# Kernel optimization log

Hardware: AMD Instinct MI355X
Metric: run time of the kernel (lower is better)

Reference implementation:

```python
import jax, jax.numpy as jnp
import numpy as np

H, E, DFF = 768, 8, 3072
B, S = 2, 1024


def setup_inputs() -> dict:
    key = jax.random.key(0)
    ks = jax.random.split(key, 4)
    scale = 1.0 / np.sqrt(H)
    return {
        "x": jax.random.normal(ks[0], (B, S, H), dtype=jnp.float32),
        "Wg": jax.random.normal(ks[1], (H, E), dtype=jnp.float32) * scale,
        "bg": jnp.zeros((E,), dtype=jnp.float32),
        "W1": jax.random.normal(ks[2], (E, H, DFF), dtype=jnp.float32) * scale,
        "b1": jnp.zeros((E, DFF), dtype=jnp.float32),
        "W2": jax.random.normal(ks[3], (E, DFF, H), dtype=jnp.float32) * (1.0 / np.sqrt(DFF)),
        "b2": jnp.zeros((E, H), dtype=jnp.float32),
        "top_k": 2,
    }


def reference(x, Wg, bg, W1, b1, W2, b2, top_k):
    b, s, h = x.shape
    xf = x.reshape(-1, h)                       # [T, H]
    logits = xf @ Wg + bg                        # [T, E]
    probs = jax.nn.softmax(logits, axis=-1)
    w, idx = jax.lax.top_k(probs, top_k)         # [T, K]
    w = w / jnp.sum(w, axis=-1, keepdims=True)   # renormalize top-k weights
    # dense combine weights per (token, expert): [T, E]
    comb = jnp.sum(jax.nn.one_hot(idx, W1.shape[0], dtype=xf.dtype) * w[..., None], axis=1)
    # per-expert MLP: Linear -> exact GELU -> Linear
    hmid = jax.nn.gelu(jnp.einsum('th,ehf->etf', xf, W1) + b1[:, None, :], approximate=False)
    eo = jnp.einsum('etf,efh->eth', hmid, W2) + b2[:, None, :]   # [E, T, H]
    out = jnp.einsum('te,eth->th', comb, eo)     # weighted combine
    return out.reshape(b, s, h)
```

## Files before the change

kernel.cpp:

```cpp
#include <hip/hip_runtime.h>
#include <hip/hip_bf16.h>
#include <math.h>

#define H_DIM 768
#define E_NUM 8
#define DFF   3072
#define T_NUM 2048
#define PAIRS 4096

typedef __attribute__((ext_vector_type(8))) short          s16x8;
typedef __attribute__((ext_vector_type(4))) float          f32x4;
typedef __attribute__((ext_vector_type(4))) unsigned int   u32x4;
typedef __attribute__((ext_vector_type(4))) unsigned short u16x4;
typedef __attribute__((ext_vector_type(8))) unsigned short u16x8;

__device__ __forceinline__ unsigned short f2bf(float f) {
  unsigned int u = __builtin_bit_cast(unsigned int, f);
  u += 0x7FFFu + ((u >> 16) & 1u);
  return (unsigned short)(u >> 16);
}

__device__ __forceinline__ float bf2f(unsigned short v) {
  unsigned int u = ((unsigned int)v) << 16;
  return __builtin_bit_cast(float, u);
}

__device__ __forceinline__ float gelu_fast(float x) {
  float t = x * x;
  float a = __builtin_fmaf(t, -0.10294221f, -2.3022082f);
  float w;
  asm("v_exp_f32 %0, %1" : "=v"(w) : "v"(x * a));
  float r;
  float d = 1.0f + w;
  asm("v_rcp_f32 %0, %1" : "=v"(r) : "v"(d));
  return x * r;
}


__device__ __forceinline__ void route_body(
    int rb, const float* __restrict__ x, const float* __restrict__ Wg,
    const float* __restrict__ bg, int* __restrict__ eidx, float* __restrict__ ew) {
  int wave = threadIdx.x >> 6, lane = threadIdx.x & 63;
  int t = rb * 4 + wave;
  const float* xr = x + (size_t)t * H_DIM;
  float acc[E_NUM];
#pragma unroll
  for (int e = 0; e < E_NUM; ++e) acc[e] = 0.f;
#pragma unroll
  for (int i = 0; i < H_DIM / 64; ++i) {
    int h = i * 64 + lane;
    float xv = xr[h];
    f32x4 w0 = *(const f32x4*)&Wg[h * 8];
    f32x4 w1 = *(const f32x4*)&Wg[h * 8 + 4];
    acc[0] += xv * w0[0]; acc[1] += xv * w0[1];
    acc[2] += xv * w0[2]; acc[3] += xv * w0[3];
    acc[4] += xv * w1[0]; acc[5] += xv * w1[1];
    acc[6] += xv * w1[2]; acc[7] += xv * w1[3];
  }
#pragma unroll
  for (int e = 0; e < E_NUM; ++e) {
#pragma unroll
    for (int off = 32; off > 0; off >>= 1) acc[e] += __shfl_xor(acc[e], off);
  }
  if (lane == 0) {
    float l[E_NUM];
#pragma unroll
    for (int e = 0; e < E_NUM; ++e) l[e] = acc[e] + bg[e];
    int i0 = 0;
#pragma unroll
    for (int e = 1; e < E_NUM; ++e) if (l[e] > l[i0]) i0 = e;
    int i1 = (i0 == 0) ? 1 : 0;
#pragma unroll
    for (int e = 0; e < E_NUM; ++e) if (e != i0 && l[e] > l[i1]) i1 = e;
    float d  = expf(l[i1] - l[i0]);
    eidx[2 * t]     = i0;
    eidx[2 * t + 1] = i1;
    ew[2 * t]       = 1.f / (1.f + d);
    ew[2 * t + 1]   = d / (1.f + d);
  }
}

__device__ __forceinline__ void transpose_body(
    int tb, const float* __restrict__ in, unsigned short* __restrict__ out,
    int R, int C) {
  __shared__ unsigned short tile[128][136];
  int tpe = (R / 128) * (C / 128);
  int e   = tb / tpe;
  int rem = tb % tpe;
  int bx  = rem % (C / 128);
  int by  = rem / (C / 128);
  int c0 = bx * 128, r0 = by * 128;
  const float* ip = in + (size_t)e * R * C;
  unsigned short* op = out + (size_t)e * R * C;
  int tid = threadIdx.x;

  int tx = tid & 31, ty = tid >> 5;
#pragma unroll
  for (int i = 0; i < 16; ++i) {
    int r = i * 8 + ty;
    f32x4 v = *(const f32x4*)&ip[(size_t)(r0 + r) * C + c0 + tx * 4];
    u16x4 o;
    o[0] = f2bf(v[0]); o[1] = f2bf(v[1]); o[2] = f2bf(v[2]); o[3] = f2bf(v[3]);
    int cs = (tx * 4) ^ (((r >> 3) & 7) << 2);
    *(u16x4*)&tile[r][cs] = o;
  }
  __syncthreads();

  int rb2 = (tid & 15) * 8;
  int key = (tid & 7) << 2;
#pragma unroll
  for (int p = 0; p < 8; ++p) {
    int c = p * 16 + (tid >> 4);
    int cs = c ^ key;
    u16x8 o;
#pragma unroll
    for (int j = 0; j < 8; ++j) o[j] = tile[rb2 + j][cs];
    *(u16x8*)&op[(size_t)(c0 + c) * R + r0 + rb2] = o;
  }
}


__global__ __launch_bounds__(256) void k_prep(
    const float* __restrict__ x, const float* __restrict__ Wg,
    const float* __restrict__ bg, int* __restrict__ eidx, float* __restrict__ ew,
    const float* __restrict__ W1, unsigned short* __restrict__ Wb1,
    const float* __restrict__ W2, unsigned short* __restrict__ Wb2) {
  constexpr int NR  = T_NUM / 4;
  constexpr int NT1 = E_NUM * (H_DIM / 128) * (DFF / 128);
  int b = blockIdx.x;
  if (b < NR)            route_body(b, x, Wg, bg, eidx, ew);
  else if (b < NR + NT1) transpose_body(b - NR, W1, Wb1, H_DIM, DFF);
  else                   transpose_body(b - NR - NT1, W2, Wb2, DFF, H_DIM);
}

__global__ __launch_bounds__(256) void k_build(
    const int* __restrict__ eidx, int* __restrict__ counts, int* __restrict__ offsets,
    int* __restrict__ tok_of, int* __restrict__ slot_of) {
  __shared__ int cnt[E_NUM];
  __shared__ int cur[E_NUM];
  int tid = threadIdx.x;
  if (tid < E_NUM) cnt[tid] = 0;
  __syncthreads();
#pragma unroll
  for (int i = 0; i < PAIRS / 256; ++i)
    atomicAdd(&cnt[eidx[i * 256 + tid]], 1);
  __syncthreads();
  if (tid == 0) {
    int s = 0;
    for (int e = 0; e < E_NUM; ++e) { cur[e] = s; s += cnt[e]; }
  }
  __syncthreads();
  if (tid < E_NUM) { counts[tid] = cnt[tid]; offsets[tid] = cur[tid]; }
#pragma unroll
  for (int i = 0; i < PAIRS / 256; ++i) {
    int p = i * 256 + tid;
    int s = atomicAdd(&cur[eidx[p]], 1);
    tok_of[s] = p >> 1;
    slot_of[p] = s;
  }
}

__global__ __launch_bounds__(256) void k_gather(
    const float* __restrict__ x, const int* __restrict__ tok_of,
    unsigned short* __restrict__ Xg) {
  int wave = threadIdx.x >> 6, lane = threadIdx.x & 63;
#pragma unroll
  for (int j = 0; j < 4; ++j) {
    int s = blockIdx.x * 16 + j * 4 + wave;
    int t = tok_of[s];
    const f32x4* xr = (const f32x4*)(x + (size_t)t * H_DIM);
    u16x4* orow = (u16x4*)(Xg + (size_t)s * H_DIM);
#pragma unroll
    for (int i = 0; i < H_DIM / 256; ++i) {
      f32x4 v = xr[i * 64 + lane];
      u16x4 o;
      o[0] = f2bf(v[0]); o[1] = f2bf(v[1]); o[2] = f2bf(v[2]); o[3] = f2bf(v[3]);
      orow[i * 64 + lane] = o;
    }
  }
}

template <int KTOT, int NT, int NSPLIT, int MT_MAX, bool GELU_OUT>
__global__ __launch_bounds__(256) void k_gemm(
    const unsigned short* __restrict__ A, const unsigned short* __restrict__ B,
    const float* __restrict__ bias, void* __restrict__ C,
    const int* __restrict__ counts, const int* __restrict__ offsets) {
  constexpr int NDIM  = NT * 128;
  constexpr int KLEN  = KTOT / NSPLIT;
  constexpr int NSTEP = KLEN / 64;
  int l = blockIdx.x;
  int nt = l % NT;  l /= NT;
  int e  = l & 7;   l >>= 3;
  int part = l % NSPLIT;
  int mt = l / NSPLIT;
  int Me = counts[e];
  if (mt * 128 >= Me) return;
  int seg = offsets[e];

  __shared__ __align__(16) unsigned short Al[2][128 * 64];
  __shared__ __align__(16) unsigned short Bl[2][128 * 64];

  int tid  = threadIdx.x;
  int lane = tid & 63;
  int wave = tid >> 6;
  int wm = wave >> 1, wn = wave & 1;

  int sr   = tid >> 3;
  int scl  = (tid & 7) * 8;
  int scs  = (((tid & 7) ^ (sr & 7)) * 8);
  int rxor = (lane & 7) << 3;

  f32x4 acc[4][4];
#pragma unroll
  for (int m = 0; m < 4; ++m)
#pragma unroll
    for (int n = 0; n < 4; ++n) acc[m][n] = (f32x4){0.f, 0.f, 0.f, 0.f};

  const unsigned short* Abase = A + (size_t)seg * KTOT;
  const unsigned short* Bbase = B + (size_t)e * NDIM * KTOT + (size_t)(nt * 128) * KTOT;
  const int kbeg = part * KLEN;

  auto stage = [&](int bb, int k0) {
#pragma unroll
    for (int j = 0; j < 4; ++j) {
      int row = j * 32 + sr;
      int r = mt * 128 + row;
      r = (r < Me) ? r : (Me - 1);
      const unsigned short* gp = Abase + (size_t)r * KTOT + k0 + scs;
      __builtin_amdgcn_global_load_lds(
          (__attribute__((address_space(1))) void*)gp,
          (__attribute__((address_space(3))) void*)&Al[bb][row * 64 + scl], 16, 0, 0);
    }
#pragma unroll
    for (int j = 0; j < 4; ++j) {
      int row = j * 32 + sr;
      const unsigned short* gp = Bbase + (size_t)row * KTOT + k0 + scs;
      __builtin_amdgcn_global_load_lds(
          (__attribute__((address_space(1))) void*)gp,
          (__attribute__((address_space(3))) void*)&Bl[bb][row * 64 + scl], 16, 0, 0);
    }
  };

  auto compute = [&](int bb) {
#pragma unroll
    for (int kk = 0; kk < 2; ++kk) {
      int ko = kk * 32 + (lane >> 4) * 8;
      s16x8 af[4], bfr[4];
#pragma unroll
      for (int m = 0; m < 4; ++m) {
        int row = wm * 64 + m * 16 + (lane & 15);
        u32x4 v = *(const u32x4*)&Al[bb][(row * 64 + ko) ^ rxor];
        af[m] = __builtin_bit_cast(s16x8, v);
      }
#pragma unroll
      for (int n = 0; n < 4; ++n) {
        int row = wn * 64 + n * 16 + (lane & 15);
        u32x4 v = *(const u32x4*)&Bl[bb][(row * 64 + ko) ^ rxor];
        bfr[n] = __builtin_bit_cast(s16x8, v);
      }
#pragma unroll
      for (int m = 0; m < 4; ++m)
#pragma unroll
        for (int n = 0; n < 4; ++n)
          acc[m][n] = __builtin_amdgcn_mfma_f32_16x16x32_bf16(af[m], bfr[n], acc[m][n], 0, 0, 0);
    }
  };

  stage(0, kbeg);
  stage(1, kbeg + 64);
  int cur = 0;
#pragma unroll
  for (int s = 0; s < NSTEP; ++s) {
    if (s + 1 < NSTEP) asm volatile("s_waitcnt vmcnt(8)" ::: "memory");
    else               asm volatile("s_waitcnt vmcnt(0)" ::: "memory");
    __builtin_amdgcn_s_barrier();
    compute(cur);
    if (s + 2 < NSTEP) {
      __builtin_amdgcn_s_barrier();
      stage(cur, kbeg + (s + 2) * 64);
    }
    cur ^= 1;
  }

  int rbase = mt * 128 + wm * 64;
  int cbase = nt * 128 + wn * 64;
#pragma unroll
  for (int m = 0; m < 4; ++m) {
#pragma unroll
    for (int n = 0; n < 4; ++n) {
      int col = cbase + n * 16 + (lane & 15);
      float bv = GELU_OUT ? bias[e * NDIM + col] : 0.f;
#pragma unroll
      for (int r = 0; r < 4; ++r) {
        int row = rbase + m * 16 + (lane >> 4) * 4 + r;
        if (row < Me) {
          float v = acc[m][n][r] + bv;
          size_t idx = ((size_t)part * PAIRS + seg + row) * NDIM + col;
          if constexpr (GELU_OUT) {
            ((unsigned short*)C)[idx] = f2bf(gelu_fast(v));
          } else {
            ((unsigned short*)C)[idx] = f2bf(v);
          }
        }
      }
    }
  }
}

template <int NSPLIT>
__global__ void k_combine(const unsigned short* __restrict__ P, const int* __restrict__ slot_of,
                          const int* __restrict__ eidx, const float* __restrict__ ew,
                          const float* __restrict__ b2, float* __restrict__ out) {
  int t = blockIdx.x;
  int i = threadIdx.x;
  int s0 = slot_of[2 * t], s1 = slot_of[2 * t + 1];
  int e0 = eidx[2 * t],    e1 = eidx[2 * t + 1];
  float w0 = ew[2 * t], w1 = ew[2 * t + 1];
  f32x4 a = *(const f32x4*)&b2[e0 * H_DIM + i * 4];
  f32x4 c = *(const f32x4*)&b2[e1 * H_DIM + i * 4];
#pragma unroll
  for (int p = 0; p < NSPLIT; ++p) {
    u16x4 va = *(const u16x4*)&P[((size_t)p * PAIRS + s0) * H_DIM + i * 4];
    u16x4 vb = *(const u16x4*)&P[((size_t)p * PAIRS + s1) * H_DIM + i * 4];
#pragma unroll
    for (int j = 0; j < 4; ++j) { a[j] += bf2f(va[j]); c[j] += bf2f(vb[j]); }
  }
  f32x4 o;
  o[0] = w0 * a[0] + w1 * c[0];
  o[1] = w0 * a[1] + w1 * c[1];
  o[2] = w0 * a[2] + w1 * c[2];
  o[3] = w0 * a[3] + w1 * c[3];
  ((f32x4*)(out + (size_t)t * H_DIM))[i] = o;
}

extern "C" void kernel_launch(void* const* d_in, const int* in_sizes, int n_in,
                              void* d_out, int out_size, void* d_ws, size_t ws_size,
                              hipStream_t stream) {
  (void)in_sizes; (void)n_in; (void)out_size;
  const float* x  = (const float*)d_in[0];
  const float* Wg = (const float*)d_in[1];
  const float* bg = (const float*)d_in[2];
  const float* W1 = (const float*)d_in[3];
  const float* b1 = (const float*)d_in[4];
  const float* W2 = (const float*)d_in[5];
  const float* b2 = (const float*)d_in[6];
  float* out = (float*)d_out;

  char* w = (char*)d_ws;
  size_t off = 0;
  auto take = [&](size_t n) { void* p = w + off; off = (off + n + 255) & ~(size_t)255; return p; };
  int*   ctrl    = (int*)  take(64 * sizeof(int));
  int*   eidx    = (int*)  take(PAIRS * sizeof(int));
  float* ew      = (float*)take(PAIRS * sizeof(float));
  int*   slot_of = (int*)  take(PAIRS * sizeof(int));
  int*   tok_of  = (int*)  take(PAIRS * sizeof(int));
  unsigned short* Xg   = (unsigned short*)take((size_t)PAIRS * H_DIM * 2);
  unsigned short* Hmid = (unsigned short*)take((size_t)PAIRS * DFF * 2);
  unsigned short* P    = (unsigned short*)take((size_t)2 * PAIRS * H_DIM * 2);
  unsigned short* Wb1  = (unsigned short*)take((size_t)E_NUM * H_DIM * DFF * 2);
  unsigned short* Wb2  = (unsigned short*)take((size_t)E_NUM * H_DIM * DFF * 2);
  if (off > ws_size) return;

  int* counts  = ctrl;
  int* offsets = ctrl + 8;

  k_prep<<<T_NUM / 4 + 2 * E_NUM * (H_DIM / 128) * (DFF / 128), 256, 0, stream>>>(
      x, Wg, bg, eidx, ew, W1, Wb1, W2, Wb2);
  k_build<<<1, 256, 0, stream>>>(eidx, counts, offsets, tok_of, slot_of);
  k_gather<<<PAIRS / 16, 256, 0, stream>>>(x, tok_of, Xg);

  k_gemm<H_DIM, DFF / 128, 1, 6, true><<<(DFF / 128) * E_NUM * 6, 256, 0, stream>>>(
      Xg, Wb1, b1, Hmid, counts, offsets);

  k_gemm<DFF, H_DIM / 128, 2, 6, false><<<(H_DIM / 128) * E_NUM * 2 * 6, 256, 0, stream>>>(
      Hmid, Wb2, b2, P, counts, offsets);
  k_combine<2><<<T_NUM, 192, 0, stream>>>(P, slot_of, eidx, ew, b2, out);
}
```

Before: 138.9 us.

## Load expert weight fragments directly from global into registers, bypassing LDS

The B (expert weight) operand is no longer staged through shared memory; each lane loads its MFMA fragments directly from global memory into double-buffered registers, with A still staged via global_load_lds. This halves LDS usage and removes the LDS reads for B, which could raise occupancy. The cost is uncoalesced 16-byte strided global loads, duplicated across the two wm waves, plus extra VGPR pressure from two register buffers, and the vmcnt accounting has to change to match.

```diff
diff --git a/kernel.cpp b/kernel.cpp
--- a/kernel.cpp
+++ b/kernel.cpp
@@ -198,7 +198,6 @@
   int seg = offsets[e];
 
   __shared__ __align__(16) unsigned short Al[2][128 * 64];
-  __shared__ __align__(16) unsigned short Bl[2][128 * 64];
 
   int tid  = threadIdx.x;
   int lane = tid & 63;
@@ -217,7 +216,8 @@
     for (int n = 0; n < 4; ++n) acc[m][n] = (f32x4){0.f, 0.f, 0.f, 0.f};
 
   const unsigned short* Abase = A + (size_t)seg * KTOT;
-  const unsigned short* Bbase = B + (size_t)e * NDIM * KTOT + (size_t)(nt * 128) * KTOT;
+  const unsigned short* Bfrag = B + (size_t)e * NDIM * KTOT
+      + (size_t)(nt * 128 + wn * 64 + (lane & 15)) * KTOT + ((lane >> 4) * 8);
   const int kbeg = part * KLEN;
 
   auto stage = [&](int bb, int k0) {
@@ -231,21 +231,23 @@
           (__attribute__((address_space(1))) void*)gp,
           (__attribute__((address_space(3))) void*)&Al[bb][row * 64 + scl], 16, 0, 0);
     }
-#pragma unroll
-    for (int j = 0; j < 4; ++j) {
-      int row = j * 32 + sr;
-      const unsigned short* gp = Bbase + (size_t)row * KTOT + k0 + scs;
-      __builtin_amdgcn_global_load_lds(
-          (__attribute__((address_space(1))) void*)gp,
-          (__attribute__((address_space(3))) void*)&Bl[bb][row * 64 + scl], 16, 0, 0);
-    }
   };
 
-  auto compute = [&](int bb) {
+  auto loadB = [&](s16x8 (&br)[4][2], int k0) {
+#pragma unroll
+    for (int n = 0; n < 4; ++n)
+#pragma unroll
+      for (int kk = 0; kk < 2; ++kk) {
+        u32x4 v = *(const u32x4*)(Bfrag + (size_t)(n * 16) * KTOT + k0 + kk * 32);
+        br[n][kk] = __builtin_bit_cast(s16x8, v);
+      }
+  };
+
+  auto compute = [&](int bb, s16x8 (&br)[4][2]) {
 #pragma unroll
     for (int kk = 0; kk < 2; ++kk) {
       int ko = kk * 32 + (lane >> 4) * 8;
-      s16x8 af[4], bfr[4];
+      s16x8 af[4];
 #pragma unroll
       for (int m = 0; m < 4; ++m) {
         int row = wm * 64 + m * 16 + (lane & 15);
@@ -253,33 +255,28 @@
         af[m] = __builtin_bit_cast(s16x8, v);
       }
 #pragma unroll
-      for (int n = 0; n < 4; ++n) {
-        int row = wn * 64 + n * 16 + (lane & 15);
-        u32x4 v = *(const u32x4*)&Bl[bb][(row * 64 + ko) ^ rxor];
-        bfr[n] = __builtin_bit_cast(s16x8, v);
-      }
-#pragma unroll
       for (int m = 0; m < 4; ++m)
 #pragma unroll
         for (int n = 0; n < 4; ++n)
-          acc[m][n] = __builtin_amdgcn_mfma_f32_16x16x32_bf16(af[m], bfr[n], acc[m][n], 0, 0, 0);
+          acc[m][n] = __builtin_amdgcn_mfma_f32_16x16x32_bf16(af[m], br[n][kk], acc[m][n], 0, 0, 0);
     }
   };
 
-  stage(0, kbeg);
-  stage(1, kbeg + 64);
-  int cur = 0;
+  s16x8 br0[4][2], br1[4][2];
+  stage(0, kbeg);       loadB(br0, kbeg);
+  stage(1, kbeg + 64);  loadB(br1, kbeg + 64);
 #pragma unroll
   for (int s = 0; s < NSTEP; ++s) {
-    if (s + 1 < NSTEP) asm volatile("s_waitcnt vmcnt(8)" ::: "memory");
+    if (s + 1 < NSTEP) asm volatile("s_waitcnt vmcnt(12)" ::: "memory");
     else               asm volatile("s_waitcnt vmcnt(0)" ::: "memory");
     __builtin_amdgcn_s_barrier();
-    compute(cur);
+    if (s & 1) compute(1, br1); else compute(0, br0);
     if (s + 2 < NSTEP) {
       __builtin_amdgcn_s_barrier();
-      stage(cur, kbeg + (s + 2) * 64);
-    }
-    cur ^= 1;
+      stage(s & 1, kbeg + (s + 2) * 64);
+      if (s & 1) loadB(br1, kbeg + (s + 2) * 64);
+      else       loadB(br0, kbeg + (s + 2) * 64);
+    }
   }
 
   int rbase = mt * 128 + wm * 64;
```

Measured after the change: 182.7 us. +31.5%, slower.
